# Kernel optimization log

Measured on AMD Instinct MI355X. Metric: run time of the kernel, lower is better.

## Reference

```python
import jax, jax.numpy as jnp
import numpy as np

N_HEADS = 16
THETA = 10000.0

def rotate_half(x):
    x1, x2 = jnp.split(x, 2, axis=-1)
    return jnp.concatenate((-x2, x1), axis=-1)

def setup_inputs() -> dict:
    key = jax.random.key(0)
    k1, k2, k3 = jax.random.split(key, 3)
    B, T, C = 4, 2048, 2048
    x = jax.random.normal(k1, (B, T, C), dtype=jnp.float32)
    # torch Linear weights: y = x @ W.T
    wqkv = jax.random.normal(k2, (3 * C, C), dtype=jnp.float32) * (1.0 / np.sqrt(C))
    w_out = jax.random.normal(k3, (C, C), dtype=jnp.float32) * (1.0 / np.sqrt(C))
    return {"x": x, "wqkv": wqkv, "w_out": w_out}

def reference(x, wqkv, w_out):
    B, T, C = x.shape
    H = N_HEADS
    hd = C // H
    scale = 1.0 / np.sqrt(hd)

    qkv = x @ wqkv.T                               # [B, T, 3C]
    q, k, v = jnp.split(qkv, 3, axis=-1)
    q = q.reshape(B, T, H, hd).transpose(0, 2, 1, 3)  # [B, H, T, hd]
    k = k.reshape(B, T, H, hd).transpose(0, 2, 1, 3)
    v = v.reshape(B, T, H, hd).transpose(0, 2, 1, 3)

    # rotary embedding (kv_len == T, no cache)
    inv_freq = 1.0 / (THETA ** (jnp.arange(0, hd, 2, dtype=jnp.float32) / hd))
    t = jnp.arange(T, dtype=jnp.float32)
    freqs = jnp.einsum("i,j->ij", t, inv_freq)     # [T, hd/2]
    emb = jnp.concatenate((freqs, freqs), axis=-1) # [T, hd]
    cos = jnp.cos(emb)[None, None, :, :]
    sin = jnp.sin(emb)[None, None, :, :]
    q = q * cos + rotate_half(q) * sin
    k = k * cos + rotate_half(k) * sin

    scores = jnp.einsum("bhqd,bhkd->bhqk", q, k) * scale
    causal = jnp.triu(jnp.ones((T, T), dtype=bool), k=1)
    scores = jnp.where(causal[None, None], -jnp.inf, scores)
    attn = jax.nn.softmax(scores, axis=-1)
    out = jnp.einsum("bhqk,bhkd->bhqd", attn, v)   # [B, H, T, hd]
    out = out.transpose(0, 2, 1, 3).reshape(B, T, C)
    output = out @ w_out.T
    return (output, k, v)
```

## Files before the change

kernel.cpp:

```cpp
#include <hip/hip_runtime.h>

#define B_ 4
#define T_ 2048
#define C_ 2048
#define H_ 16
#define HD_ 128
#define BT_ (B_*T_)
#define N3_ (3*C_)

typedef unsigned short u16;
typedef unsigned int u32;
using short8 = __attribute__((ext_vector_type(8))) short;
using f32x4  = __attribute__((ext_vector_type(4))) float;

__device__ __forceinline__ u16 f2bf(float f) {
  union { float f; u32 u; } v; v.f = f;
  u32 r = v.u + 0x7FFFu + ((v.u >> 16) & 1u);
  return (u16)(r >> 16);
}
__device__ __forceinline__ float bf2f(u16 u) {
  union { u32 u; float f; } v; v.u = ((u32)u) << 16;
  return v.f;
}
__device__ __forceinline__ void gload_lds16(const void* g, void* l) {
  __builtin_amdgcn_global_load_lds((const __attribute__((address_space(1))) void*)g,
                                   (__attribute__((address_space(3))) void*)l, 16, 0, 0);
}

__global__ __launch_bounds__(256) void cast_f2b_kernel(const float* __restrict__ in,
                                                       u16* __restrict__ out, int n4) {
  int i = blockIdx.x * 256 + threadIdx.x;
  if (i >= n4) return;
  float4 v = ((const float4*)in)[i];
  ushort4 o;
  o.x = f2bf(v.x); o.y = f2bf(v.y); o.z = f2bf(v.z); o.w = f2bf(v.w);
  ((ushort4*)out)[i] = o;
}

__global__ __launch_bounds__(256) void rope_table_kernel(float* __restrict__ cosb,
                                                         float* __restrict__ sinb) {
  int i = blockIdx.x * 256 + threadIdx.x;
  int t = i >> 6, d = i & 63;
  float inv = powf(10000.0f, -(float)d / 64.0f);
  float ang = (float)t * inv;
  cosb[i] = cosf(ang);
  sinb[i] = sinf(ang);
}

template<int MODE>
__global__ __launch_bounds__(512, 2) void gemm3p_kernel(const u16* __restrict__ A,
    const u16* __restrict__ Bw, void* __restrict__ Cout, int M, int N, int K, int ntx,
    u16* __restrict__ qb, u16* __restrict__ kbb, float* __restrict__ kout,
    float* __restrict__ vout, u16* __restrict__ vtb,
    const float* __restrict__ cosb, const float* __restrict__ sinb) {
  extern __shared__ u16 ldsx[];
  int lin = blockIdx.x;
  int x = lin & 7, q = lin >> 3;
  int j = q & 31, rr = q >> 5;
  int rid = rr * 8 + x;
  int rgn = ntx >> 2;
  int rmr = rid / rgn, rnr = rid - rmr * rgn;
  int mtile = rmr * 8 + (j >> 2);
  int ntile = rnr * 4 + (j & 3);
  int tid = threadIdx.x, w = tid >> 6, l = tid & 63;
  int lr = l & 15, lg = l >> 4;
  int wr = w >> 2, wc = w & 3;
  const u16* Abase = A + (size_t)mtile * 256 * K;
  const u16* Bbase = Bw + (size_t)ntile * 256 * K;

  int srow[2], scol[2], sdst[2];
  #pragma unroll
  for (int jj = 0; jj < 2; ++jj) {
    int s = jj*512 + tid;
    srow[jj] = (s >> 6)*8 + (s & 7);
    scol[jj] = ((s >> 3) & 7) * 8;
    sdst[jj] = s * 8;
  }
  int arow[8], brow[4];
  #pragma unroll
  for (int mi = 0; mi < 8; ++mi) {
    int rho = mi*16 + lr;
    arow[mi] = (rho >> 3)*512 + (rho & 7)*8 + lg*64;
  }
  #pragma unroll
  for (int nj = 0; nj < 4; ++nj) {
    int rho = (wc & 1)*64 + nj*16 + lr;
    brow[nj] = (rho >> 3)*512 + (rho & 7)*8 + lg*64;
  }
  const int haOff = (2 + wr) * 8192;
  const int hbOff = (wc >> 1) * 8192;

  auto stageB = [&](int Tp) {
    u16* dst = ldsx + (Tp & 1) * 32768;
    const u16* g = Bbase + Tp * 64;
    #pragma unroll
    for (int jj = 0; jj < 2; ++jj)
      gload_lds16(g + (size_t)srow[jj] * K + scol[jj], dst + sdst[jj]);
    #pragma unroll
    for (int jj = 0; jj < 2; ++jj)
      gload_lds16(g + (size_t)(128 + srow[jj]) * K + scol[jj], dst + 8192 + sdst[jj]);
  };
  auto stageA = [&](int Tp) {
    u16* dst = ldsx + (Tp & 1) * 32768 + 16384;
    const u16* g = Abase + Tp * 64;
    #pragma unroll
    for (int jj = 0; jj < 2; ++jj)
      gload_lds16(g + (size_t)srow[jj] * K + scol[jj], dst + sdst[jj]);
    #pragma unroll
    for (int jj = 0; jj < 2; ++jj)
      gload_lds16(g + (size_t)(128 + srow[jj]) * K + scol[jj], dst + 8192 + sdst[jj]);
  };

  short8 am03[4][2], am47[4][2], bn01[2][2], bn23[2][2];
  auto readQ0 = [&](int T) {
    const u16* base = ldsx + (T & 1) * 32768;
    #pragma unroll
    for (int i = 0; i < 4; ++i)
      #pragma unroll
      for (int kk = 0; kk < 2; ++kk)
        am03[i][kk] = *(const short8*)(base + haOff + arow[i] + kk*256);
    #pragma unroll
    for (int jj = 0; jj < 2; ++jj)
      #pragma unroll
      for (int kk = 0; kk < 2; ++kk)
        bn01[jj][kk] = *(const short8*)(base + hbOff + brow[jj] + kk*256);
  };

  f32x4 acc[8][4];
  #pragma unroll
  for (int mi = 0; mi < 8; ++mi)
    #pragma unroll
    for (int n = 0; n < 4; ++n) acc[mi][n] = (f32x4){0.f,0.f,0.f,0.f};

  const int NT = K >> 6;
  stageB(0); stageA(0); stageB(1); stageA(1);
  asm volatile("s_waitcnt vmcnt(8)" ::: "memory");
  __builtin_amdgcn_sched_barrier(0);
  __builtin_amdgcn_s_barrier();
  readQ0(0);

  for (int T = 0; T < NT; ++T) {
    const u16* base = ldsx + (T & 1) * 32768;
    bool stg = (T + 2) < NT;
    #pragma unroll
    for (int jj = 0; jj < 2; ++jj)
      #pragma unroll
      for (int kk = 0; kk < 2; ++kk)
        bn23[jj][kk] = *(const short8*)(base + hbOff + brow[2+jj] + kk*256);
    __builtin_amdgcn_s_barrier();
    __builtin_amdgcn_s_setprio(1);
    #pragma unroll
    for (int i = 0; i < 4; ++i)
      #pragma unroll
      for (int jj = 0; jj < 2; ++jj)
        #pragma unroll
        for (int kk = 0; kk < 2; ++kk)
          acc[i][jj] = __builtin_amdgcn_mfma_f32_16x16x32_bf16(am03[i][kk], bn01[jj][kk], acc[i][jj], 0, 0, 0);
    __builtin_amdgcn_s_setprio(0);
    __builtin_amdgcn_s_barrier();
    if (stg) stageB(T + 2);
    #pragma unroll
    for (int i = 0; i < 4; ++i)
      #pragma unroll
      for (int kk = 0; kk < 2; ++kk)
        am47[i][kk] = *(const short8*)(base + haOff + arow[4+i] + kk*256);
    __builtin_amdgcn_s_barrier();
    __builtin_amdgcn_s_setprio(1);
    #pragma unroll
    for (int i = 0; i < 4; ++i)
      #pragma unroll
      for (int jj = 0; jj < 2; ++jj)
        #pragma unroll
        for (int kk = 0; kk < 2; ++kk)
          acc[i][2+jj] = __builtin_amdgcn_mfma_f32_16x16x32_bf16(am03[i][kk], bn23[jj][kk], acc[i][2+jj], 0, 0, 0);
    __builtin_amdgcn_s_setprio(0);
    __builtin_amdgcn_s_barrier();
    if (stg) {
      stageA(T + 2);
      asm volatile("s_waitcnt vmcnt(8)" ::: "memory");
    } else {
      asm volatile("s_waitcnt vmcnt(0)" ::: "memory");
    }
    __builtin_amdgcn_sched_barrier(0);
    __builtin_amdgcn_s_barrier();
    __builtin_amdgcn_s_setprio(1);
    #pragma unroll
    for (int i = 0; i < 4; ++i)
      #pragma unroll
      for (int jj = 0; jj < 2; ++jj)
        #pragma unroll
        for (int kk = 0; kk < 2; ++kk)
          acc[4+i][2+jj] = __builtin_amdgcn_mfma_f32_16x16x32_bf16(am47[i][kk], bn23[jj][kk], acc[4+i][2+jj], 0, 0, 0);
    #pragma unroll
    for (int i = 0; i < 4; ++i)
      #pragma unroll
      for (int jj = 0; jj < 2; ++jj)
        #pragma unroll
        for (int kk = 0; kk < 2; ++kk)
          acc[4+i][jj] = __builtin_amdgcn_mfma_f32_16x16x32_bf16(am47[i][kk], bn01[jj][kk], acc[4+i][jj], 0, 0, 0);
    __builtin_amdgcn_s_setprio(0);
    if (T + 1 < NT) readQ0(T + 1);
    __builtin_amdgcn_s_barrier();
  }

  if (MODE == 0) {
    #pragma unroll
    for (int mi = 0; mi < 8; ++mi)
      #pragma unroll
      for (int n = 0; n < 4; ++n)
        #pragma unroll
        for (int r = 0; r < 4; ++r) {
          int grow = mtile*256 + wr*128 + mi*16 + lg*4 + r;
          int gcol = ntile*256 + wc*64 + n*16 + lr;
          ((float*)Cout)[(size_t)grow * N + gcol] = acc[mi][n][r];
        }
  } else {
    const float SCALE = 0.08838834764831845f;
    u16* eld = ldsx;
    int btype = ntile >> 3;
    int colg0 = ntile * 256;
    #pragma unroll 1
    for (int h = 0; h < 2; ++h) {
      __builtin_amdgcn_s_barrier();
      if (wr == h) {
        #pragma unroll
        for (int mi = 0; mi < 8; ++mi)
          #pragma unroll
          for (int n = 0; n < 4; ++n)
            #pragma unroll
            for (int r = 0; r < 4; ++r) {
              int row = mi*16 + lg*4 + r;
              int col = wc*64 + n*16 + lr;
              eld[row*256 + col] = f2bf(acc[mi][n][r]);
            }
      }
      __builtin_amdgcn_s_barrier();
      int grow0 = mtile*256 + h*128;
      if (btype < 2) {
        #pragma unroll 1
        for (int ps = 0; ps < 8; ++ps) {
          int ch = ps*512 + tid;
          int row = ch >> 5, c8 = (ch & 31) * 8;
          int grow = grow0 + row;
          int t = grow & 2047, bb = grow >> 11;
          int cq = colg0 + c8 - btype*2048;
          int hh = cq >> 7;
          float vals[8];
          #pragma unroll
          for (int e = 0; e < 8; ++e) {
            int c = c8 + e;
            int dloc = c & 127;
            int dd = dloc & 63;
            float cs = cosb[t*64 + dd], sn = sinb[t*64 + dd];
            float x0 = bf2f(eld[row*256 + c]);
            float x1 = bf2f(eld[row*256 + (c ^ 64)]);
            vals[e] = (dloc < 64) ? (x0*cs - x1*sn) : (x0*cs + x1*sn);
          }
          size_t obase = ((size_t)(bb*16 + hh)*2048 + t)*128 + (cq & 127);
          if (btype == 0) {
            short8 pk;
            #pragma unroll
            for (int e = 0; e < 8; ++e) pk[e] = (short)f2bf(vals[e]*SCALE);
            *(short8*)(qb + obase) = pk;
          } else {
            short8 pk;
            #pragma unroll
            for (int e = 0; e < 8; ++e) pk[e] = (short)f2bf(vals[e]);
            *(short8*)(kbb + obase) = pk;
            float4 f0 = {vals[0], vals[1], vals[2], vals[3]};
            float4 f1 = {vals[4], vals[5], vals[6], vals[7]};
            *(float4*)(kout + obase) = f0;
            *(float4*)(kout + obase + 4) = f1;
          }
        }
      } else {
        #pragma unroll 1
        for (int ps = 0; ps < 8; ++ps) {
          int ch = ps*512 + tid;
          int row = ch >> 5, c8 = (ch & 31) * 8;
          int grow = grow0 + row;
          int t = grow & 2047, bb = grow >> 11;
          int cv = colg0 + c8 - 4096;
          int hh = cv >> 7;
          size_t obase = ((size_t)(bb*16 + hh)*2048 + t)*128 + (cv & 127);
          float4 f0, f1;
          #pragma unroll
          for (int e = 0; e < 4; ++e) f0[e] = bf2f(eld[row*256 + c8 + e]);
          #pragma unroll
          for (int e = 0; e < 4; ++e) f1[e] = bf2f(eld[row*256 + c8 + 4 + e]);
          *(float4*)(vout + obase) = f0;
          *(float4*)(vout + obase + 4) = f1;
        }
        #pragma unroll 1
        for (int ps = 0; ps < 8; ++ps) {
          int ch = ps*512 + tid;
          int c = ch >> 4, rg = (ch & 15) * 8;
          int cv = colg0 + c - 4096;
          int hh = cv >> 7, dd = cv & 127;
          int grow = grow0 + rg;
          int t0 = grow & 2047, bb = grow >> 11;
          short8 pk;
          #pragma unroll
          for (int e = 0; e < 8; ++e) pk[e] = (short)eld[(rg + e)*256 + c];
          *(short8*)(vtb + ((size_t)(bb*16 + hh)*128 + dd)*2048 + t0) = pk;
        }
      }
    }
  }
}

struct TileSt {
  short8 aq[4];
  f32x4 oacc[8];
  float m_run[4];
  float l_run[4];
};

__device__ __forceinline__ void stage_kv(const u16* kpl, const u16* vpl, int kt,
                                         u16* Kd, u16* Vd, int w, int l) {
  const u16* kTile = kpl + (size_t)kt * 64 * HD_;
  int ktOff = kt * 64;
  #pragma unroll
  for (int j = 0; j < 4; ++j) {
    int s = (j*4 + w)*64 + l;
    int g = s ^ ((s >> 4) & 7);
    gload_lds16(kTile + (g >> 4)*HD_ + (g & 15)*8, (char*)Kd + (j*4 + w)*1024);
    int g2 = s ^ ((s >> 3) & 7);
    gload_lds16(vpl + (size_t)(g2 >> 3)*T_ + ktOff + (g2 & 7)*8, (char*)Vd + (j*4 + w)*1024);
  }
}

__device__ __forceinline__ void attn_tile(TileSt& st, const u16* Kl, const u16* Vl,
                                          char* Pw, bool diag, int lr, int lg, int w) {
  f32x4 s_acc[4];
  #pragma unroll
  for (int ct = 0; ct < 4; ++ct) s_acc[ct] = (f32x4){0.f, 0.f, 0.f, 0.f};
  __builtin_amdgcn_s_setprio(1);
  #pragma unroll
  for (int kg = 0; kg < 4; ++kg) {
    #pragma unroll
    for (int ct = 0; ct < 4; ++ct) {
      int krow = ct*16 + lr;
      int kbyte = (krow*256 + (kg*32 + lg*8)*2) ^ ((krow & 7) << 4);
      short8 bk = *(const short8*)((const char*)Kl + kbyte);
      s_acc[ct] = __builtin_amdgcn_mfma_f32_16x16x32_bf16(st.aq[kg], bk, s_acc[ct], 0, 0, 0);
    }
  }
  __builtin_amdgcn_s_setprio(0);
  float p[4][4];
  #pragma unroll
  for (int ct = 0; ct < 4; ++ct)
    #pragma unroll
    for (int r = 0; r < 4; ++r) {
      float sv = s_acc[ct][r];
      if (diag && (ct*16 + lr) > (w*16 + lg*4 + r)) sv = -INFINITY;
      p[ct][r] = sv;
    }
  float fac[4];
  #pragma unroll
  for (int r = 0; r < 4; ++r) {
    float mx = fmaxf(fmaxf(p[0][r], p[1][r]), fmaxf(p[2][r], p[3][r]));
    #pragma unroll
    for (int off = 1; off < 16; off <<= 1) mx = fmaxf(mx, __shfl_xor(mx, off));
    float mn = fmaxf(st.m_run[r], mx);
    fac[r] = __expf(st.m_run[r] - mn);
    st.m_run[r] = mn;
    float ls = 0.f;
    #pragma unroll
    for (int ct = 0; ct < 4; ++ct) { float pv = __expf(p[ct][r] - mn); p[ct][r] = pv; ls += pv; }
    #pragma unroll
    for (int off = 1; off < 16; off <<= 1) ls += __shfl_xor(ls, off);
    st.l_run[r] = st.l_run[r] * fac[r] + ls;
  }
  #pragma unroll
  for (int dt = 0; dt < 8; ++dt)
    #pragma unroll
    for (int r = 0; r < 4; ++r) st.oacc[dt][r] *= fac[r];
  #pragma unroll
  for (int ct = 0; ct < 4; ++ct)
    #pragma unroll
    for (int r = 0; r < 4; ++r) {
      int prow = lg*4 + r;
      int pb = (prow*128 + (ct*16 + lr)*2) ^ ((prow & 7) << 4);
      *(u16*)(Pw + pb) = f2bf(p[ct][r]);
    }
  asm volatile("s_waitcnt lgkmcnt(0)" ::: "memory");
  __builtin_amdgcn_sched_barrier(0);
  short8 pa[2];
  #pragma unroll
  for (int kk = 0; kk < 2; ++kk) {
    int pb = (lr*128 + (kk*32 + lg*8)*2) ^ ((lr & 7) << 4);
    pa[kk] = *(const short8*)(Pw + pb);
  }
  __builtin_amdgcn_s_setprio(1);
  #pragma unroll
  for (int dt = 0; dt < 8; ++dt) {
    #pragma unroll
    for (int kk = 0; kk < 2; ++kk) {
      int vrow = dt*16 + lr;
      int vbyte = (vrow*128 + (kk*32 + lg*8)*2) ^ ((vrow & 7) << 4);
      short8 bv = *(const short8*)((const char*)Vl + vbyte);
      st.oacc[dt] = __builtin_amdgcn_mfma_f32_16x16x32_bf16(pa[kk], bv, st.oacc[dt], 0, 0, 0);
    }
  }
  __builtin_amdgcn_s_setprio(0);
}

__device__ __forceinline__ void write_out(TileSt& st, u16* __restrict__ ao,
                                          int b, int h, int qbase, int lr, int lg, int w) {
  float invl[4];
  #pragma unroll
  for (int r = 0; r < 4; ++r) invl[r] = 1.0f / st.l_run[r];
  #pragma unroll
  for (int dt = 0; dt < 8; ++dt)
    #pragma unroll
    for (int r = 0; r < 4; ++r) {
      int t = qbase + w*16 + lg*4 + r;
      int col = h*HD_ + dt*16 + lr;
      ao[(size_t)(b * T_ + t) * C_ + col] = f2bf(st.oacc[dt][r] * invl[r]);
    }
}

__global__ __launch_bounds__(256, 2) void attn_kernel(const u16* __restrict__ qb,
    const u16* __restrict__ kb, const u16* __restrict__ vtb, u16* __restrict__ ao) {
  __shared__ u16 Kl[2][64 * 128];
  __shared__ u16 Vl[2][128 * 64];
  __shared__ u16 Pl[4][16 * 64];
  int bid0 = blockIdx.x;
  int bid = (bid0 & 7) * 128 + (bid0 >> 3);
  int bh = bid >> 4, pr = bid & 15;
  int lo = pr, hi = 31 - pr;
  int b = bh >> 4, h = bh & 15;
  int tid = threadIdx.x, w = tid >> 6, l = tid & 63;
  int lr = l & 15, lg = l >> 4;
  const u16* qptr = qb + (size_t)bh * T_ * HD_;
  const u16* kpl  = kb + (size_t)bh * T_ * HD_;
  const u16* vpl  = vtb + (size_t)bh * HD_ * T_;
  char* Pw = (char*)&Pl[w][0];

  TileSt stL, stH;
  #pragma unroll
  for (int kg = 0; kg < 4; ++kg) {
    stL.aq[kg] = *(const short8*)(qptr + (size_t)(lo*64 + w*16 + lr) * HD_ + kg*32 + lg*8);
    stH.aq[kg] = *(const short8*)(qptr + (size_t)(hi*64 + w*16 + lr) * HD_ + kg*32 + lg*8);
  }
  #pragma unroll
  for (int dt = 0; dt < 8; ++dt) {
    stL.oacc[dt] = (f32x4){0.f, 0.f, 0.f, 0.f};
    stH.oacc[dt] = (f32x4){0.f, 0.f, 0.f, 0.f};
  }
  #pragma unroll
  for (int r = 0; r < 4; ++r) {
    stL.m_run[r] = -INFINITY; stH.m_run[r] = -INFINITY;
    stL.l_run[r] = 0.f;       stH.l_run[r] = 0.f;
  }

  stage_kv(kpl, vpl, 0, &Kl[0][0], &Vl[0][0], w, l);
  __syncthreads();
  int cur = 0;
  for (int kt = 0; kt <= hi; ++kt) {
    if (kt < hi) stage_kv(kpl, vpl, kt + 1, &Kl[cur ^ 1][0], &Vl[cur ^ 1][0], w, l);
    attn_tile(stH, &Kl[cur][0], &Vl[cur][0], Pw, kt == hi, lr, lg, w);
    if (kt <= lo) attn_tile(stL, &Kl[cur][0], &Vl[cur][0], Pw, kt == lo, lr, lg, w);
    __syncthreads();
    cur ^= 1;
  }
  write_out(stH, ao, b, h, hi*64, lr, lg, w);
  write_out(stL, ao, b, h, lo*64, lr, lg, w);
}

extern "C" void kernel_launch(void* const* d_in, const int* in_sizes, int n_in,
                              void* d_out, int out_size, void* d_ws, size_t ws_size,
                              hipStream_t stream) {
  const float* x     = (const float*)d_in[0];
  const float* wqkv  = (const float*)d_in[1];
  const float* w_out = (const float*)d_in[2];
  float* out = (float*)d_out;

  char* ws = (char*)d_ws;
  size_t off = 0;
  u16* xb    = (u16*)(ws + off); off += (size_t)BT_ * C_ * 2;
  u16* wqkvb = (u16*)(ws + off); off += (size_t)N3_ * C_ * 2;
  u16* woutb = (u16*)(ws + off); off += (size_t)C_ * C_ * 2;
  u16* qbf   = (u16*)(ws + off); off += (size_t)BT_ * C_ * 2;
  u16* aob   = (u16*)(ws + off); off += (size_t)BT_ * C_ * 2;
  u16* kbb   = (u16*)(ws + off); off += (size_t)BT_ * C_ * 2;
  u16* vtb   = (u16*)(ws + off); off += (size_t)BT_ * C_ * 2;
  float* cosb = (float*)(ws + off); off += (size_t)T_ * 64 * 4;
  float* sinb = (float*)(ws + off); off += (size_t)T_ * 64 * 4;

  float* kout = out + (size_t)BT_ * C_;
  float* vout = out + 2 * (size_t)BT_ * C_;

  hipFuncSetAttribute((const void*)gemm3p_kernel<1>,
                      hipFuncAttributeMaxDynamicSharedMemorySize, 131072);
  hipFuncSetAttribute((const void*)gemm3p_kernel<0>,
                      hipFuncAttributeMaxDynamicSharedMemorySize, 131072);

  cast_f2b_kernel<<<(BT_*C_/4)/256, 256, 0, stream>>>(x, xb, BT_*C_/4);
  cast_f2b_kernel<<<(N3_*C_/4)/256, 256, 0, stream>>>(wqkv, wqkvb, N3_*C_/4);
  cast_f2b_kernel<<<(C_*C_/4)/256, 256, 0, stream>>>(w_out, woutb, C_*C_/4);
  rope_table_kernel<<<(T_*64)/256, 256, 0, stream>>>(cosb, sinb);
  gemm3p_kernel<1><<<(N3_/256)*(BT_/256), 512, 131072, stream>>>(
      xb, wqkvb, nullptr, BT_, N3_, C_, N3_/256,
      qbf, kbb, kout, vout, vtb, cosb, sinb);
  attn_kernel<<<B_*H_*16, 256, 0, stream>>>(qbf, kbb, vtb, aob);
  gemm3p_kernel<0><<<(C_/256)*(BT_/256), 512, 131072, stream>>>(
      aob, woutb, out, BT_, C_, C_, C_/256,
      nullptr, nullptr, nullptr, nullptr, nullptr, nullptr, nullptr);
}
```

Baseline: 642.0 us.

## Move V transpose into separate kernel and write V directly from accumulators

For V tiles, the QKV GEMM epilogue now writes the fp32 V output and a bf16 copy straight from the accumulator registers, with no LDS staging. A new vt_kernel then transposes the bf16 V into the layout the attention kernel reads. The Q/K epilogue pads LDS rows to 264 elements and reads eight values with vector LDS loads. This is meant to cut LDS bank conflicts and remove the slow strided transpose from the GEMM tail, at the cost of an extra launch and an extra round trip of V through global memory.

```diff
diff --git a/kernel.cpp b/kernel.cpp
--- a/kernel.cpp
+++ b/kernel.cpp
@@ -47,11 +47,39 @@
   sinb[i] = sinf(ang);
 }
 
+__global__ __launch_bounds__(256) void vt_kernel(const u16* __restrict__ vb,
+                                                 u16* __restrict__ vtb) {
+  __shared__ u16 tile[64][72];
+  int bid = blockIdx.x;
+  int dh = bid & 1, tt = (bid >> 1) & 31, bh = bid >> 6;
+  int tid = threadIdx.x;
+  int tr = tid >> 2, tc = tid & 3;
+  const u16* src = vb + ((size_t)bh*2048 + tt*64 + tr)*128 + dh*64 + tc*16;
+  short8 v0 = *(const short8*)src;
+  short8 v1 = *(const short8*)(src + 8);
+  #pragma unroll
+  for (int j = 0; j < 8; ++j) {
+    tile[tr][tc*16 + j]     = (u16)v0[j];
+    tile[tr][tc*16 + 8 + j] = (u16)v1[j];
+  }
+  __syncthreads();
+  int dr = tid >> 2, c2 = tid & 3;
+  short8 o0, o1;
+  #pragma unroll
+  for (int j = 0; j < 8; ++j) {
+    o0[j] = (short)tile[c2*16 + j][dr];
+    o1[j] = (short)tile[c2*16 + 8 + j][dr];
+  }
+  u16* dst = vtb + ((size_t)bh * HD_ + dh*64 + dr) * T_ + tt*64 + c2*16;
+  *(short8*)dst = o0;
+  *(short8*)(dst + 8) = o1;
+}
+
 template<int MODE>
 __global__ __launch_bounds__(512, 2) void gemm3p_kernel(const u16* __restrict__ A,
     const u16* __restrict__ Bw, void* __restrict__ Cout, int M, int N, int K, int ntx,
     u16* __restrict__ qb, u16* __restrict__ kbb, float* __restrict__ kout,
-    float* __restrict__ vout, u16* __restrict__ vtb,
+    float* __restrict__ vout, u16* __restrict__ vb,
     const float* __restrict__ cosb, const float* __restrict__ sinb) {
   extern __shared__ u16 ldsx[];
   int lin = blockIdx.x;
@@ -219,24 +247,41 @@
     u16* eld = ldsx;
     int btype = ntile >> 3;
     int colg0 = ntile * 256;
-    #pragma unroll 1
-    for (int h = 0; h < 2; ++h) {
-      __builtin_amdgcn_s_barrier();
-      if (wr == h) {
+    if (btype == 2) {
+      #pragma unroll
+      for (int mi = 0; mi < 8; ++mi)
         #pragma unroll
-        for (int mi = 0; mi < 8; ++mi)
+        for (int n = 0; n < 4; ++n)
           #pragma unroll
-          for (int n = 0; n < 4; ++n)
+          for (int r = 0; r < 4; ++r) {
+            int grow = mtile*256 + wr*128 + mi*16 + lg*4 + r;
+            int gcol = colg0 + wc*64 + n*16 + lr;
+            int t = grow & 2047, bb = grow >> 11;
+            int cv = gcol - 4096;
+            int hh = cv >> 7, dd = cv & 127;
+            size_t o = ((size_t)(bb*16 + hh)*2048 + t)*128 + dd;
+            float v = acc[mi][n][r];
+            vout[o] = v;
+            vb[o] = f2bf(v);
+          }
+    } else {
+      #pragma unroll 1
+      for (int h = 0; h < 2; ++h) {
+        __syncthreads();
+        if (wr == h) {
+          #pragma unroll
+          for (int mi = 0; mi < 8; ++mi)
             #pragma unroll
-            for (int r = 0; r < 4; ++r) {
-              int row = mi*16 + lg*4 + r;
-              int col = wc*64 + n*16 + lr;
-              eld[row*256 + col] = f2bf(acc[mi][n][r]);
-            }
-      }
-      __builtin_amdgcn_s_barrier();
-      int grow0 = mtile*256 + h*128;
-      if (btype < 2) {
+            for (int n = 0; n < 4; ++n)
+              #pragma unroll
+              for (int r = 0; r < 4; ++r) {
+                int row = mi*16 + lg*4 + r;
+                int col = wc*64 + n*16 + lr;
+                eld[row*264 + col] = f2bf(acc[mi][n][r]);
+              }
+        }
+        __syncthreads();
+        int grow0 = mtile*256 + h*128;
         #pragma unroll 1
         for (int ps = 0; ps < 8; ++ps) {
           int ch = ps*512 + tid;
@@ -244,19 +289,20 @@
           int grow = grow0 + row;
           int t = grow & 2047, bb = grow >> 11;
           int cq = colg0 + c8 - btype*2048;
-          int hh = cq >> 7;
+          int hh = cq >> 7, dloc = cq & 127;
+          int dd0 = dloc & 63;
+          short8 x0 = *(const short8*)(eld + row*264 + c8);
+          short8 x1 = *(const short8*)(eld + row*264 + (c8 ^ 64));
           float vals[8];
           #pragma unroll
           for (int e = 0; e < 8; ++e) {
-            int c = c8 + e;
-            int dloc = c & 127;
-            int dd = dloc & 63;
-            float cs = cosb[t*64 + dd], sn = sinb[t*64 + dd];
-            float x0 = bf2f(eld[row*256 + c]);
-            float x1 = bf2f(eld[row*256 + (c ^ 64)]);
-            vals[e] = (dloc < 64) ? (x0*cs - x1*sn) : (x0*cs + x1*sn);
+            float cs = cosb[t*64 + dd0 + e];
+            float sn = sinb[t*64 + dd0 + e];
+            float a0 = bf2f((u16)x0[e]);
+            float a1 = bf2f((u16)x1[e]);
+            vals[e] = (dloc < 64) ? (a0*cs - a1*sn) : (a0*cs + a1*sn);
           }
-          size_t obase = ((size_t)(bb*16 + hh)*2048 + t)*128 + (cq & 127);
+          size_t obase = ((size_t)(bb*16 + hh)*2048 + t)*128 + dloc;
           if (btype == 0) {
             short8 pk;
             #pragma unroll
@@ -273,37 +319,6 @@
             *(float4*)(kout + obase + 4) = f1;
           }
         }
-      } else {
-        #pragma unroll 1
-        for (int ps = 0; ps < 8; ++ps) {
-          int ch = ps*512 + tid;
-          int row = ch >> 5, c8 = (ch & 31) * 8;
-          int grow = grow0 + row;
-          int t = grow & 2047, bb = grow >> 11;
-          int cv = colg0 + c8 - 4096;
-          int hh = cv >> 7;
-          size_t obase = ((size_t)(bb*16 + hh)*2048 + t)*128 + (cv & 127);
-          float4 f0, f1;
-          #pragma unroll
-          for (int e = 0; e < 4; ++e) f0[e] = bf2f(eld[row*256 + c8 + e]);
-          #pragma unroll
-          for (int e = 0; e < 4; ++e) f1[e] = bf2f(eld[row*256 + c8 + 4 + e]);
-          *(float4*)(vout + obase) = f0;
-          *(float4*)(vout + obase + 4) = f1;
-        }
-        #pragma unroll 1
-        for (int ps = 0; ps < 8; ++ps) {
-          int ch = ps*512 + tid;
-          int c = ch >> 4, rg = (ch & 15) * 8;
-          int cv = colg0 + c - 4096;
-          int hh = cv >> 7, dd = cv & 127;
-          int grow = grow0 + rg;
-          int t0 = grow & 2047, bb = grow >> 11;
-          short8 pk;
-          #pragma unroll
-          for (int e = 0; e < 8; ++e) pk[e] = (short)eld[(rg + e)*256 + c];
-          *(short8*)(vtb + ((size_t)(bb*16 + hh)*128 + dd)*2048 + t0) = pk;
-        }
       }
     }
   }
@@ -486,6 +501,7 @@
   u16* aob   = (u16*)(ws + off); off += (size_t)BT_ * C_ * 2;
   u16* kbb   = (u16*)(ws + off); off += (size_t)BT_ * C_ * 2;
   u16* vtb   = (u16*)(ws + off); off += (size_t)BT_ * C_ * 2;
+  u16* vb    = (u16*)(ws + off); off += (size_t)BT_ * C_ * 2;
   float* cosb = (float*)(ws + off); off += (size_t)T_ * 64 * 4;
   float* sinb = (float*)(ws + off); off += (size_t)T_ * 64 * 4;
 
@@ -503,7 +519,8 @@
   rope_table_kernel<<<(T_*64)/256, 256, 0, stream>>>(cosb, sinb);
   gemm3p_kernel<1><<<(N3_/256)*(BT_/256), 512, 131072, stream>>>(
       xb, wqkvb, nullptr, BT_, N3_, C_, N3_/256,
-      qbf, kbb, kout, vout, vtb, cosb, sinb);
+      qbf, kbb, kout, vout, vb, cosb, sinb);
+  vt_kernel<<<B_*H_*(T_/64)*2, 256, 0, stream>>>(vb, vtb);
   attn_kernel<<<B_*H_*16, 256, 0, stream>>>(qbf, kbb, vtb, aob);
   gemm3p_kernel<0><<<(C_/256)*(BT_/256), 512, 131072, stream>>>(
       aob, woutb, out, BT_, C_, C_, C_/256,
```

New measurement: 600.5 us. -6.5%, faster.
